# Kernel tuning notes

Measured on AMD Instinct MI355X. Metric: run time of the kernel, lower is better.

The kernel has to match this reference:

```python
import jax
import jax.numpy as jnp
import numpy as np
import math

B, FRAMES, TLEN, E = 16, 8192, 512, 256
DUR = FRAMES // TLEN  # frames per phone


def setup_inputs() -> dict:
    key = jax.random.key(0)
    ks = jax.random.split(key, 8)
    encoder_out = jax.random.normal(ks[0], (B, TLEN, E), dtype=jnp.float32)
    # consecutively-distinct phone ids so the aligner advances exactly once per phone
    text_phone = jnp.broadcast_to(jnp.arange(TLEN, dtype=jnp.int32) % 97 + 1, (B, TLEN))
    align_phone = jnp.repeat(text_phone, DUR, axis=1)  # [B, FRAMES]
    pitch = jax.random.normal(ks[1], (B, FRAMES, 1), dtype=jnp.float32)
    beats = jax.random.randint(ks[2], (B, FRAMES, 1), 0, 2, dtype=jnp.int32)
    s = 1.0 / math.sqrt(E)
    fc_pitch_w = jax.random.normal(ks[3], (E, 1), dtype=jnp.float32)
    fc_pitch_b = jax.random.normal(ks[4], (E,), dtype=jnp.float32) * 0.01
    fc_pos_w = jax.random.normal(ks[5], (E, E), dtype=jnp.float32) * s
    fc_pos_b = jax.random.normal(ks[6], (E,), dtype=jnp.float32) * 0.01
    emb_beats = jax.random.normal(ks[7], (2, E), dtype=jnp.float32)
    return {"encoder_out": encoder_out, "align_phone": align_phone,
            "text_phone": text_phone, "pitch": pitch, "beats": beats,
            "fc_pitch_w": fc_pitch_w, "fc_pitch_b": fc_pitch_b,
            "fc_pos_w": fc_pos_w, "fc_pos_b": fc_pos_b, "emb_beats": emb_beats}


def _align_indices(ap, tp):
    """Replicates the eager aligner: ind_j = ind_{j-1} + (ap[j] != tp[ind_{j-1}]).
    ap: [FRAMES] int, tp: [TLEN] int -> [FRAMES] int32 gather indices."""
    tlen = tp.shape[0]

    def step(ind, a):
        new_ind = jnp.where(a == tp[ind], ind, jnp.minimum(ind + 1, tlen - 1))
        return new_ind, new_ind

    _, inds = jax.lax.scan(step, jnp.int32(0), ap[1:])
    return jnp.concatenate([jnp.zeros((1,), jnp.int32), inds])


def _positional_encoding(frames, d_model, dtype=jnp.float32):
    pos = jnp.arange(frames, dtype=jnp.float32)[:, None]            # [F,1]
    div = jnp.exp(jnp.arange(0, d_model, 2, dtype=jnp.float32) * (-math.log(10000.0) / d_model))
    pe = jnp.zeros((frames, d_model), dtype=jnp.float32)
    pe = pe.at[:, 0::2].set(jnp.sin(pos * div))
    pe = pe.at[:, 1::2].set(jnp.cos(pos * div))
    return pe.astype(dtype)


def reference(encoder_out, align_phone, text_phone, pitch, beats,
              fc_pitch_w, fc_pitch_b, fc_pos_w, fc_pos_b, emb_beats):
    # duration regulator: gather encoder states per frame  -> [B, FRAMES, E]
    inds = jax.vmap(_align_indices)(align_phone, text_phone)           # [B, FRAMES]
    aligner_out = jnp.take_along_axis(encoder_out, inds[..., None], axis=1)
    # pitch linear (in_features=1)
    pitch_proj = jnp.einsum('bfo,eo->bfe', pitch, fc_pitch_w) + fc_pitch_b
    # beats embedding
    beat_emb = emb_beats[beats[..., 0]]                                # [B, FRAMES, E]
    # positional encoding + fc_pos (PE added to aligner_out, dropout = identity)
    pe = _positional_encoding(aligner_out.shape[1], aligner_out.shape[2],
                              aligner_out.dtype)                        # [FRAMES, E]
    pos_out = jnp.einsum('bfe,de->bfd', aligner_out + pe[None], fc_pos_w) + fc_pos_b
    return aligner_out + pitch_proj + beat_emb + pos_out
```

## Files before the change

### kernel.cpp

```cpp
#include <hip/hip_runtime.h>
#include <hip/hip_bf16.h>

#define BATCH 16
#define FRAMES 8192
#define TLEN 512
#define EDIM 256
#define SP 56

typedef __attribute__((ext_vector_type(8))) short short8;
typedef __attribute__((ext_vector_type(4))) float f32x4;

__device__ __forceinline__ unsigned cvt2(float lo, float hi) {
    __hip_bfloat162 t = __float22bfloat162_rn(make_float2(lo, hi));
    return *reinterpret_cast<unsigned*>(&t);
}
__device__ __forceinline__ unsigned long long pack4(f32x4 u) {
    return (unsigned long long)cvt2(u[0], u[1]) |
           ((unsigned long long)cvt2(u[2], u[3]) << 32);
}

__global__ __launch_bounds__(512) void k_prep(const float* __restrict__ X,
                                              const float* __restrict__ W,
                                              const float* __restrict__ pos_b,
                                              const float* __restrict__ pit_b,
                                              const int* __restrict__ ap,
                                              const int* __restrict__ tp,
                                              float* __restrict__ G,
                                              float* __restrict__ Q,
                                              int* __restrict__ inds) {
    __shared__ short lds[(64 + 256) * SP];
    int bid = blockIdx.x;
    int tid = threadIdx.x;

    if (bid >= 240) {
        int b = bid - 240;
        int* tps = (int*)lds;
        int* wsum = tps + TLEN;
        int* okp = wsum + 8;
        const int* apb = ap + b * FRAMES;
        tps[tid] = tp[b * TLEN + tid];
        if (tid == 0) *okp = 1;
        __syncthreads();
        int j0 = tid * 16;
        int4 v0 = ((const int4*)apb)[tid * 4];
        int4 v1 = ((const int4*)apb)[tid * 4 + 1];
        int4 v2 = ((const int4*)apb)[tid * 4 + 2];
        int4 v3 = ((const int4*)apb)[tid * 4 + 3];
        int a[16] = {v0.x, v0.y, v0.z, v0.w, v1.x, v1.y, v1.z, v1.w,
                     v2.x, v2.y, v2.z, v2.w, v3.x, v3.y, v3.z, v3.w};
        int pr = (tid == 0) ? a[0] : apb[j0 - 1];
        int c = 0, p[16];
#pragma unroll
        for (int k = 0; k < 16; ++k) {
            c += ((j0 + k) > 0) && (a[k] != pr);
            p[k] = c;
            pr = a[k];
        }
        int lane = tid & 63, wv = tid >> 6;
        int sc = c;
#pragma unroll
        for (int d = 1; d < 64; d <<= 1) {
            int o = __shfl_up(sc, d);
            if (lane >= d) sc += o;
        }
        if (lane == 63) wsum[wv] = sc;
        __syncthreads();
        int wbase = 0;
        for (int w = 0; w < wv; ++w) wbase += wsum[w];
        int excl = wbase + sc - c;
        int g[16];
#pragma unroll
        for (int k = 0; k < 16; ++k) g[k] = min(excl + p[k], TLEN - 1);
        int4* ob = (int4*)(inds + b * FRAMES);
#pragma unroll
        for (int q4 = 0; q4 < 4; ++q4) {
            int4 wv4;
            wv4.x = g[q4 * 4]; wv4.y = g[q4 * 4 + 1];
            wv4.z = g[q4 * 4 + 2]; wv4.w = g[q4 * 4 + 3];
            ob[tid * 4 + q4] = wv4;
        }
        int ok = 1, gp = min(excl, TLEN - 1);
#pragma unroll
        for (int k = 0; k < 16; ++k) {
            int j = j0 + k, e;
            if (j == 0) e = 0;
            else e = (a[k] == tps[gp]) ? gp : min(gp + 1, TLEN - 1);
            ok &= (g[k] == e);
            gp = g[k];
        }
        if (!ok) atomicAnd(okp, 0);
        __syncthreads();
        if (*okp == 0 && tid == 0) {
            int ind = 0, cur = tps[0];
            int* o = inds + b * FRAMES;
            o[0] = 0;
            for (int j = 1; j < FRAMES; ++j) {
                int aj = apb[j];
                if (aj != cur && ind < TLEN - 1) { ind++; cur = tps[ind]; }
                o[j] = ind;
            }
        }
    }

    int qmode = (bid >= 128);
    int row0 = (qmode ? bid - 128 : bid) * 64;
    short* Xs = lds;
    short* Ws = lds + 64 * SP;
    int lane = tid & 63, wv = tid >> 6;
    int c = lane & 15, gq = lane >> 4;
    int r0 = (wv & 3) * 16, cc0 = (wv >> 2) * 128;
    int sr = tid >> 3, spart = tid & 7;
    f32x4 acc[8];
#pragma unroll
    for (int i = 0; i < 8; ++i) acc[i] = (f32x4){0.f, 0.f, 0.f, 0.f};

    const float kPE = -0.03597789207803197f;
    const float INV2PI = 0.15915494309189535f;

    for (int ks = 0; ks < 8; ++ks) {
        int k0 = ks * 32;
        __syncthreads();
        {
            unsigned long long pk;
            if (!qmode) {
                f32x4 u = *(const f32x4*)(X + (row0 + sr) * EDIM + k0 + spart * 4);
                pk = pack4(u);
            } else {
                float fr = (float)(row0 + sr);
                int e0 = k0 + spart * 4;
                float dv0 = __expf((float)e0 * kPE);
                float dv1 = __expf((float)(e0 + 2) * kPE);
                float a0 = fr * dv0 * INV2PI; a0 -= floorf(a0);
                float a1 = fr * dv1 * INV2PI; a1 -= floorf(a1);
                f32x4 v;
                v[0] = __builtin_amdgcn_sinf(a0);
                v[1] = __builtin_amdgcn_cosf(a0);
                v[2] = __builtin_amdgcn_sinf(a1);
                v[3] = __builtin_amdgcn_cosf(a1);
                pk = pack4(v);
            }
            *((unsigned long long*)&Xs[sr * SP + spart * 4]) = pk;
        }
#pragma unroll
        for (int m = 0; m < 4; ++m) {
            int d = sr + 64 * m;
            f32x4 u = *(const f32x4*)(W + d * EDIM + k0 + spart * 4);
            if (!qmode) {
#pragma unroll
                for (int j = 0; j < 4; ++j)
                    if (d == k0 + spart * 4 + j) u[j] += 1.0f;
            }
            *((unsigned long long*)&Ws[d * SP + spart * 4]) = pack4(u);
        }
        __syncthreads();
        short8 af = *((const short8*)&Xs[(r0 + c) * SP + gq * 8]);
#pragma unroll
        for (int tc = 0; tc < 8; ++tc) {
            short8 bf = *((const short8*)&Ws[(cc0 + tc * 16 + c) * SP + gq * 8]);
            acc[tc] = __builtin_amdgcn_mfma_f32_16x16x32_bf16(af, bf, acc[tc], 0, 0, 0);
        }
    }
    int mrow = row0 + r0 + gq * 4;
    if (!qmode) {
#pragma unroll
        for (int tc = 0; tc < 8; ++tc) {
            int d = cc0 + tc * 16 + c;
#pragma unroll
            for (int i = 0; i < 4; ++i)
                G[(mrow + i) * EDIM + d] = acc[tc][i];
        }
    } else {
#pragma unroll
        for (int tc = 0; tc < 8; ++tc) {
            int d = cc0 + tc * 16 + c;
            float bb = pos_b[d] + pit_b[d];
#pragma unroll
            for (int i = 0; i < 4; ++i)
                Q[(mrow + i) * EDIM + d] = acc[tc][i] + bb;
        }
    }
}

__global__ __launch_bounds__(256) void k_final(const float* __restrict__ G,
                                               const float* __restrict__ Q,
                                               const int* __restrict__ inds,
                                               const float* __restrict__ pitch,
                                               const int* __restrict__ beats,
                                               const float* __restrict__ wp,
                                               const float* __restrict__ eb,
                                               float* __restrict__ out) {
    int swz = (blockIdx.x & 7) * 256 + (blockIdx.x >> 3);
    int f0 = swz * 4;
    int wv = threadIdx.x >> 6, lane = threadIdx.x & 63;
    f32x4 w4 = ((const f32x4*)wp)[lane];
    f32x4 e0 = ((const f32x4*)eb)[lane];
    f32x4 e1 = ((const f32x4*)eb)[64 + lane];
    f32x4 q[4];
#pragma unroll
    for (int f = 0; f < 4; ++f) q[f] = ((const f32x4*)Q)[(f0 + f) * 64 + lane];
#pragma unroll
    for (int bg = 0; bg < 1; ++bg) {
        ;
    }
#pragma unroll
    for (int bb = 0; bb < 4; ++bb) {
        int b = wv * 4 + bb;
        int idx0 = b * FRAMES + f0;
        int4 iv = *(const int4*)(inds + idx0);
        f32x4 pv4 = *(const f32x4*)(pitch + idx0);
        int4 tv = *(const int4*)(beats + idx0);
        int indv[4] = {iv.x, iv.y, iv.z, iv.w};
        float pv[4] = {pv4[0], pv4[1], pv4[2], pv4[3]};
        int btv[4] = {tv.x, tv.y, tv.z, tv.w};
#pragma unroll
        for (int f = 0; f < 4; ++f) {
            f32x4 g = ((const f32x4*)G)[(b * TLEN + indv[f]) * 64 + lane];
            f32x4 e = btv[f] ? e1 : e0;
            f32x4 r;
#pragma unroll
            for (int i = 0; i < 4; ++i) r[i] = g[i] + q[f][i] + pv[f] * w4[i] + e[i];
            ((f32x4*)out)[(idx0 + f) * 64 + lane] = r;
        }
    }
}

extern "C" void kernel_launch(void* const* d_in, const int* in_sizes, int n_in,
                              void* d_out, int out_size, void* d_ws, size_t ws_size,
                              hipStream_t stream) {
    const float* enc   = (const float*)d_in[0];
    const int*   ap    = (const int*)d_in[1];
    const int*   tp    = (const int*)d_in[2];
    const float* pitch = (const float*)d_in[3];
    const int*   beats = (const int*)d_in[4];
    const float* wpit  = (const float*)d_in[5];
    const float* bpit  = (const float*)d_in[6];
    const float* wpos  = (const float*)d_in[7];
    const float* bpos  = (const float*)d_in[8];
    const float* ebts  = (const float*)d_in[9];
    float* out = (float*)d_out;
    char* ws = (char*)d_ws;
    int*   inds = (int*)ws;
    float* G    = (float*)(ws + (1 << 20));
    float* Q    = (float*)(ws + (9 << 20));

    hipLaunchKernelGGL(k_prep, dim3(256), dim3(512), 0, stream,
                       enc, wpos, bpos, bpit, ap, tp, G, Q, inds);
    hipLaunchKernelGGL(k_final, dim3(2048), dim3(256), 0, stream,
                       G, Q, inds, pitch, beats, wpit, ebts, out);
}
```

Measured before the change: 44.33 us.

## Fuse positional-encoding GEMM into final kernel and rebalance prep blocks

The PE-projection GEMM (Q) moves out of the prep kernel and into the final kernel. Each block now computes a 16-frame Q tile in LDS and applies it across all 16 batches, so Q is never written to or read from global memory. The prep kernel now handles only the encoder GEMM with 32-row tiles and 256-thread blocks, plus the alignment scan with 32 frames per thread. The cost is that every final block reloads the full weight matrix and runs a small MFMA GEMM, and there are fewer, larger final blocks.

Result: slower. 63.75 us (+43.8%).

```diff
diff --git a/kernel.cpp b/kernel.cpp
--- a/kernel.cpp
+++ b/kernel.cpp
@@ -19,71 +19,66 @@
            ((unsigned long long)cvt2(u[2], u[3]) << 32);
 }
 
-__global__ __launch_bounds__(512) void k_prep(const float* __restrict__ X,
-                                              const float* __restrict__ W,
-                                              const float* __restrict__ pos_b,
-                                              const float* __restrict__ pit_b,
-                                              const int* __restrict__ ap,
-                                              const int* __restrict__ tp,
-                                              float* __restrict__ G,
-                                              float* __restrict__ Q,
-                                              int* __restrict__ inds) {
-    __shared__ short lds[(64 + 256) * SP];
-    int bid = blockIdx.x;
-    int tid = threadIdx.x;
-
-    if (bid >= 240) {
-        int b = bid - 240;
+__global__ __launch_bounds__(256) void k1(const float* __restrict__ X,
+                                          const float* __restrict__ W,
+                                          const int* __restrict__ ap,
+                                          const int* __restrict__ tp,
+                                          float* __restrict__ G,
+                                          int* __restrict__ inds) {
+    __shared__ short lds[(32 + 256) * SP];
+    int bid = blockIdx.x, tid = threadIdx.x;
+
+    if (bid >= 256) {
+        int b = bid - 256;
         int* tps = (int*)lds;
         int* wsum = tps + TLEN;
-        int* okp = wsum + 8;
+        int* okp = wsum + 4;
         const int* apb = ap + b * FRAMES;
         tps[tid] = tp[b * TLEN + tid];
+        tps[tid + 256] = tp[b * TLEN + tid + 256];
         if (tid == 0) *okp = 1;
         __syncthreads();
-        int j0 = tid * 16;
-        int4 v0 = ((const int4*)apb)[tid * 4];
-        int4 v1 = ((const int4*)apb)[tid * 4 + 1];
-        int4 v2 = ((const int4*)apb)[tid * 4 + 2];
-        int4 v3 = ((const int4*)apb)[tid * 4 + 3];
-        int a[16] = {v0.x, v0.y, v0.z, v0.w, v1.x, v1.y, v1.z, v1.w,
-                     v2.x, v2.y, v2.z, v2.w, v3.x, v3.y, v3.z, v3.w};
+        int j0 = tid * 32;
+        int a[32];
+#pragma unroll
+        for (int q = 0; q < 8; ++q)
+            *(int4*)(a + q * 4) = ((const int4*)(apb + j0))[q];
         int pr = (tid == 0) ? a[0] : apb[j0 - 1];
-        int c = 0, p[16];
-#pragma unroll
-        for (int k = 0; k < 16; ++k) {
-            c += ((j0 + k) > 0) && (a[k] != pr);
-            p[k] = c;
+        int cnt = 0, p[32];
+#pragma unroll
+        for (int k = 0; k < 32; ++k) {
+            cnt += ((j0 + k) > 0) && (a[k] != pr);
+            p[k] = cnt;
             pr = a[k];
         }
-        int lane = tid & 63, wv = tid >> 6;
-        int sc = c;
+        int lane = tid & 63, wvi = tid >> 6;
+        int sc = cnt;
 #pragma unroll
         for (int d = 1; d < 64; d <<= 1) {
             int o = __shfl_up(sc, d);
             if (lane >= d) sc += o;
         }
-        if (lane == 63) wsum[wv] = sc;
+        if (lane == 63) wsum[wvi] = sc;
         __syncthreads();
         int wbase = 0;
-        for (int w = 0; w < wv; ++w) wbase += wsum[w];
-        int excl = wbase + sc - c;
-        int g[16];
-#pragma unroll
-        for (int k = 0; k < 16; ++k) g[k] = min(excl + p[k], TLEN - 1);
-        int4* ob = (int4*)(inds + b * FRAMES);
-#pragma unroll
-        for (int q4 = 0; q4 < 4; ++q4) {
-            int4 wv4;
-            wv4.x = g[q4 * 4]; wv4.y = g[q4 * 4 + 1];
-            wv4.z = g[q4 * 4 + 2]; wv4.w = g[q4 * 4 + 3];
-            ob[tid * 4 + q4] = wv4;
+        for (int w = 0; w < wvi; ++w) wbase += wsum[w];
+        int excl = wbase + sc - cnt;
+        int g[32];
+#pragma unroll
+        for (int k = 0; k < 32; ++k) g[k] = min(excl + p[k], TLEN - 1);
+        int4* ob = (int4*)(inds + b * FRAMES + j0);
+#pragma unroll
+        for (int q = 0; q < 8; ++q) {
+            int4 o4;
+            o4.x = g[q * 4]; o4.y = g[q * 4 + 1];
+            o4.z = g[q * 4 + 2]; o4.w = g[q * 4 + 3];
+            ob[q] = o4;
         }
         int ok = 1, gp = min(excl, TLEN - 1);
 #pragma unroll
-        for (int k = 0; k < 16; ++k) {
-            int j = j0 + k, e;
-            if (j == 0) e = 0;
+        for (int k = 0; k < 32; ++k) {
+            int e;
+            if (j0 + k == 0) e = 0;
             else e = (a[k] == tps[gp]) ? gp : min(gp + 1, TLEN - 1);
             ok &= (g[k] == e);
             gp = g[k];
@@ -100,56 +95,34 @@
                 o[j] = ind;
             }
         }
-    }
-
-    int qmode = (bid >= 128);
-    int row0 = (qmode ? bid - 128 : bid) * 64;
+        return;
+    }
+
+    int row0 = bid * 32;
     short* Xs = lds;
-    short* Ws = lds + 64 * SP;
+    short* Ws = lds + 32 * SP;
     int lane = tid & 63, wv = tid >> 6;
     int c = lane & 15, gq = lane >> 4;
-    int r0 = (wv & 3) * 16, cc0 = (wv >> 2) * 128;
+    int r0 = (wv & 1) * 16, cc0 = (wv >> 1) * 128;
     int sr = tid >> 3, spart = tid & 7;
     f32x4 acc[8];
 #pragma unroll
     for (int i = 0; i < 8; ++i) acc[i] = (f32x4){0.f, 0.f, 0.f, 0.f};
 
-    const float kPE = -0.03597789207803197f;
-    const float INV2PI = 0.15915494309189535f;
-
     for (int ks = 0; ks < 8; ++ks) {
         int k0 = ks * 32;
         __syncthreads();
         {
-            unsigned long long pk;
-            if (!qmode) {
-                f32x4 u = *(const f32x4*)(X + (row0 + sr) * EDIM + k0 + spart * 4);
-                pk = pack4(u);
-            } else {
-                float fr = (float)(row0 + sr);
-                int e0 = k0 + spart * 4;
-                float dv0 = __expf((float)e0 * kPE);
-                float dv1 = __expf((float)(e0 + 2) * kPE);
-                float a0 = fr * dv0 * INV2PI; a0 -= floorf(a0);
-                float a1 = fr * dv1 * INV2PI; a1 -= floorf(a1);
-                f32x4 v;
-                v[0] = __builtin_amdgcn_sinf(a0);
-                v[1] = __builtin_amdgcn_cosf(a0);
-                v[2] = __builtin_amdgcn_sinf(a1);
-                v[3] = __builtin_amdgcn_cosf(a1);
-                pk = pack4(v);
-            }
-            *((unsigned long long*)&Xs[sr * SP + spart * 4]) = pk;
-        }
-#pragma unroll
-        for (int m = 0; m < 4; ++m) {
-            int d = sr + 64 * m;
+            f32x4 u = *(const f32x4*)(X + (row0 + sr) * EDIM + k0 + spart * 4);
+            *((unsigned long long*)&Xs[sr * SP + spart * 4]) = pack4(u);
+        }
+#pragma unroll
+        for (int m = 0; m < 8; ++m) {
+            int d = sr + 32 * m;
             f32x4 u = *(const f32x4*)(W + d * EDIM + k0 + spart * 4);
-            if (!qmode) {
-#pragma unroll
-                for (int j = 0; j < 4; ++j)
-                    if (d == k0 + spart * 4 + j) u[j] += 1.0f;
-            }
+#pragma unroll
+            for (int j = 0; j < 4; ++j)
+                if (d == k0 + spart * 4 + j) u[j] += 1.0f;
             *((unsigned long long*)&Ws[d * SP + spart * 4]) = pack4(u);
         }
         __syncthreads();
@@ -161,51 +134,95 @@
         }
     }
     int mrow = row0 + r0 + gq * 4;
-    if (!qmode) {
-#pragma unroll
-        for (int tc = 0; tc < 8; ++tc) {
-            int d = cc0 + tc * 16 + c;
-#pragma unroll
-            for (int i = 0; i < 4; ++i)
-                G[(mrow + i) * EDIM + d] = acc[tc][i];
-        }
-    } else {
-#pragma unroll
-        for (int tc = 0; tc < 8; ++tc) {
-            int d = cc0 + tc * 16 + c;
-            float bb = pos_b[d] + pit_b[d];
-#pragma unroll
-            for (int i = 0; i < 4; ++i)
-                Q[(mrow + i) * EDIM + d] = acc[tc][i] + bb;
-        }
-    }
-}
-
-__global__ __launch_bounds__(256) void k_final(const float* __restrict__ G,
-                                               const float* __restrict__ Q,
-                                               const int* __restrict__ inds,
-                                               const float* __restrict__ pitch,
-                                               const int* __restrict__ beats,
-                                               const float* __restrict__ wp,
-                                               const float* __restrict__ eb,
-                                               float* __restrict__ out) {
-    int swz = (blockIdx.x & 7) * 256 + (blockIdx.x >> 3);
-    int f0 = swz * 4;
-    int wv = threadIdx.x >> 6, lane = threadIdx.x & 63;
+#pragma unroll
+    for (int tc = 0; tc < 8; ++tc) {
+        int d = cc0 + tc * 16 + c;
+#pragma unroll
+        for (int i = 0; i < 4; ++i)
+            G[(mrow + i) * EDIM + d] = acc[tc][i];
+    }
+}
+
+__global__ __launch_bounds__(256) void k2(const float* __restrict__ W,
+                                          const float* __restrict__ pos_b,
+                                          const float* __restrict__ pit_b,
+                                          const float* __restrict__ G,
+                                          const int* __restrict__ inds,
+                                          const float* __restrict__ pitch,
+                                          const int* __restrict__ beats,
+                                          const float* __restrict__ wp,
+                                          const float* __restrict__ eb,
+                                          float* __restrict__ out) {
+    __shared__ short lds[(16 + 256) * SP];
+    __shared__ float Qs[16][256];
+    int bid = blockIdx.x, tid = threadIdx.x;
+    int swz = (bid & 7) * 64 + (bid >> 3);
+    int f0 = swz * 16;
+    short* Xs = lds;
+    short* Ws = lds + 16 * SP;
+    int lane = tid & 63, wv = tid >> 6;
+    int c = lane & 15, gq = lane >> 4;
+    int cc0 = wv * 64;
+    int sr = tid >> 3, spart = tid & 7;
+    f32x4 acc[4];
+#pragma unroll
+    for (int i = 0; i < 4; ++i) acc[i] = (f32x4){0.f, 0.f, 0.f, 0.f};
+
+    const float kPE = -0.03597789207803197f;
+    const float INV2PI = 0.15915494309189535f;
+
+    for (int ks = 0; ks < 8; ++ks) {
+        int k0 = ks * 32;
+        __syncthreads();
+        if (tid < 128) {
+            int srx = tid >> 3;
+            float fr = (float)(f0 + srx);
+            int e0 = k0 + spart * 4;
+            float dv0 = __expf((float)e0 * kPE);
+            float dv1 = __expf((float)(e0 + 2) * kPE);
+            float a0 = fr * dv0 * INV2PI; a0 -= floorf(a0);
+            float a1 = fr * dv1 * INV2PI; a1 -= floorf(a1);
+            f32x4 v;
+            v[0] = __builtin_amdgcn_sinf(a0);
+            v[1] = __builtin_amdgcn_cosf(a0);
+            v[2] = __builtin_amdgcn_sinf(a1);
+            v[3] = __builtin_amdgcn_cosf(a1);
+            *((unsigned long long*)&Xs[srx * SP + spart * 4]) = pack4(v);
+        }
+#pragma unroll
+        for (int m = 0; m < 8; ++m) {
+            int d = sr + 32 * m;
+            f32x4 u = *(const f32x4*)(W + d * EDIM + k0 + spart * 4);
+            *((unsigned long long*)&Ws[d * SP + spart * 4]) = pack4(u);
+        }
+        __syncthreads();
+        short8 af = *((const short8*)&Xs[c * SP + gq * 8]);
+#pragma unroll
+        for (int tc = 0; tc < 4; ++tc) {
+            short8 bf = *((const short8*)&Ws[(cc0 + tc * 16 + c) * SP + gq * 8]);
+            acc[tc] = __builtin_amdgcn_mfma_f32_16x16x32_bf16(af, bf, acc[tc], 0, 0, 0);
+        }
+    }
+#pragma unroll
+    for (int tc = 0; tc < 4; ++tc) {
+        int d = cc0 + tc * 16 + c;
+        float bb = pos_b[d] + pit_b[d];
+#pragma unroll
+        for (int i = 0; i < 4; ++i)
+            Qs[gq * 4 + i][d] = acc[tc][i] + bb;
+    }
+    __syncthreads();
+
     f32x4 w4 = ((const f32x4*)wp)[lane];
-    f32x4 e0 = ((const f32x4*)eb)[lane];
-    f32x4 e1 = ((const f32x4*)eb)[64 + lane];
+    f32x4 e0v = ((const f32x4*)eb)[lane];
+    f32x4 e1v = ((const f32x4*)eb)[64 + lane];
+    int fw = wv * 4;
     f32x4 q[4];
 #pragma unroll
-    for (int f = 0; f < 4; ++f) q[f] = ((const f32x4*)Q)[(f0 + f) * 64 + lane];
-#pragma unroll
-    for (int bg = 0; bg < 1; ++bg) {
-        ;
-    }
-#pragma unroll
-    for (int bb = 0; bb < 4; ++bb) {
-        int b = wv * 4 + bb;
-        int idx0 = b * FRAMES + f0;
+    for (int f = 0; f < 4; ++f) q[f] = *(const f32x4*)&Qs[fw + f][lane * 4];
+#pragma unroll
+    for (int b = 0; b < BATCH; ++b) {
+        int idx0 = b * FRAMES + f0 + fw;
         int4 iv = *(const int4*)(inds + idx0);
         f32x4 pv4 = *(const f32x4*)(pitch + idx0);
         int4 tv = *(const int4*)(beats + idx0);
@@ -215,7 +232,7 @@
 #pragma unroll
         for (int f = 0; f < 4; ++f) {
             f32x4 g = ((const f32x4*)G)[(b * TLEN + indv[f]) * 64 + lane];
-            f32x4 e = btv[f] ? e1 : e0;
+            f32x4 e = btv[f] ? e1v : e0v;
             f32x4 r;
 #pragma unroll
             for (int i = 0; i < 4; ++i) r[i] = g[i] + q[f][i] + pv[f] * w4[i] + e[i];
@@ -241,10 +258,9 @@
     char* ws = (char*)d_ws;
     int*   inds = (int*)ws;
     float* G    = (float*)(ws + (1 << 20));
-    float* Q    = (float*)(ws + (9 << 20));
-
-    hipLaunchKernelGGL(k_prep, dim3(256), dim3(512), 0, stream,
-                       enc, wpos, bpos, bpit, ap, tp, G, Q, inds);
-    hipLaunchKernelGGL(k_final, dim3(2048), dim3(256), 0, stream,
-                       G, Q, inds, pitch, beats, wpit, ebts, out);
-}
+
+    hipLaunchKernelGGL(k1, dim3(272), dim3(256), 0, stream,
+                       enc, wpos, ap, tp, G, inds);
+    hipLaunchKernelGGL(k2, dim3(512), dim3(256), 0, stream,
+                       wpos, bpos, bpit, G, inds, pitch, beats, wpit, ebts, out);
+}
```
